# Kernel tuning notes

Measured on AMD Instinct MI355X. Metric: run time of the kernel, lower is better.

The kernel has to match this reference:

```python
import jax, jax.numpy as jnp
import numpy as np
from jax import lax

B, T, C = 4, 1024, 1024
NH, HD = 16, 64
SCALE = 1.0 / np.sqrt(HD)
LN_EPS = 1e-5


def _layernorm(x, g, b):
    mu = jnp.mean(x, axis=-1, keepdims=True)
    var = jnp.var(x, axis=-1, keepdims=True)
    return (x - mu) * lax.rsqrt(var + LN_EPS) * g + b


def _compress(seg, w, g, b):
    # seg: [B, nH, L, hd]; depthwise Conv1d(k=2, s=2, p=1, groups=hd, no bias) + LayerNorm(hd)
    Bs, nH, L, hd = seg.shape
    xc = seg.reshape(Bs * nH, L, hd).transpose(0, 2, 1)  # [B*nH, hd, L]
    y = lax.conv_general_dilated(xc, w, window_strides=(2,), padding=[(1, 1)],
                                 dimension_numbers=('NCH', 'OIH', 'NCH'),
                                 feature_group_count=hd)  # [B*nH, hd, L//2+1]
    y = y.transpose(0, 2, 1)
    y = _layernorm(y, g, b)
    return y.reshape(Bs, nH, -1, hd)


def setup_inputs() -> dict:
    key = jax.random.key(0)
    ks = jax.random.split(key, 16)
    d = {
        'x': jax.random.normal(ks[0], (B, T, C), jnp.float32),
        'mem_k1': jax.random.normal(ks[1], (B, NH, 129, HD), jnp.float32),
        'mem_v1': jax.random.normal(ks[2], (B, NH, 129, HD), jnp.float32),
        'mem_k2': jax.random.normal(ks[3], (B, NH, 257, HD), jnp.float32),
        'mem_v2': jax.random.normal(ks[4], (B, NH, 257, HD), jnp.float32),
        'mem_k3': jax.random.normal(ks[5], (B, NH, 513, HD), jnp.float32),
        'mem_v3': jax.random.normal(ks[6], (B, NH, 513, HD), jnp.float32),
        'c_attn_w': jax.random.normal(ks[7], (3 * C, C), jnp.float32) * 0.02,
        'c_attn_b': jnp.zeros((3 * C,), jnp.float32),
        'c_proj_w': jax.random.normal(ks[8], (C, C), jnp.float32) * 0.02,
        'c_proj_b': jnp.zeros((C,), jnp.float32),
        'compress_k_w': jax.random.normal(ks[9], (HD, 1, 2), jnp.float32) * 0.5,
        'ln_k_g': jnp.ones((HD,), jnp.float32),
        'ln_k_b': jnp.zeros((HD,), jnp.float32),
        'compress_v_w': jax.random.normal(ks[10], (HD, 1, 2), jnp.float32) * 0.5,
        'ln_v_g': jnp.ones((HD,), jnp.float32),
        'ln_v_b': jnp.zeros((HD,), jnp.float32),
    }
    return d


def reference(x, mem_k1, mem_v1, mem_k2, mem_v2, mem_k3, mem_v3,
              c_attn_w, c_attn_b, c_proj_w, c_proj_b,
              compress_k_w, ln_k_g, ln_k_b, compress_v_w, ln_v_g, ln_v_b):
    # qkv projection
    qkv = x @ c_attn_w.T + c_attn_b  # [B, T, 3C]
    q, k_new, v_new = jnp.split(qkv, 3, axis=2)
    q = q.reshape(B, T, NH, HD).transpose(0, 2, 1, 3)       # [B, nH, T, hd]
    k_new = k_new.reshape(B, T, NH, HD).transpose(0, 2, 1, 3)
    v_new = v_new.reshape(B, T, NH, HD).transpose(0, 2, 1, 3)

    # compress the most recent cached segment (513 -> 257)
    k3c = _compress(mem_k3, compress_k_w, ln_k_g, ln_k_b)
    v3c = _compress(mem_v3, compress_v_w, ln_v_g, ln_v_b)

    all_k = jnp.concatenate([mem_k1, mem_k2, k3c, k_new], axis=2)  # [B, nH, T_mem, hd]
    all_v = jnp.concatenate([mem_v1, mem_v2, v3c, v_new], axis=2)
    T_mem = all_k.shape[2]

    att = jnp.einsum('bhqd,bhkd->bhqk', q, all_k) * SCALE  # [B, nH, T, T_mem]
    # causal mask taken from tril(block_size)[:T, :T_mem]: row i attends cols j <= i
    mask = jnp.arange(T)[:, None] >= jnp.arange(T_mem)[None, :]
    att = jnp.where(mask, att, -jnp.inf)
    att = jax.nn.softmax(att, axis=-1)
    y = jnp.einsum('bhqk,bhkd->bhqd', att, all_v)  # [B, nH, T, hd]
    y = y.transpose(0, 2, 1, 3).reshape(B, T, C)
    y = y @ c_proj_w.T + c_proj_b
    return y
```

## Files before the change

### kernel.cpp

```cpp
#include <hip/hip_runtime.h>


using u16    = unsigned short;
using bf16x8 = __attribute__((ext_vector_type(8))) __bf16;
using f32x4  = __attribute__((ext_vector_type(4))) float;
using u16x8  = __attribute__((ext_vector_type(8))) unsigned short;
using u16x4  = __attribute__((ext_vector_type(4))) unsigned short;

__device__ __forceinline__ u16 f2bf(float f) {
    union { float f; unsigned u; } v; v.f = f;
    unsigned r = v.u + 0x7FFFu + ((v.u >> 16) & 1u);
    return (u16)(r >> 16);
}

__device__ __forceinline__ void gload16(const void* src, const void* lds_base) {
    __builtin_amdgcn_global_load_lds(
        (const __attribute__((address_space(1))) void*)src,
        (__attribute__((address_space(3))) void*)lds_base, 16, 0, 0);
}

__global__ void cvt_f32_bf16(const float* __restrict__ src, u16* __restrict__ dst, int n4) {
    int i = blockIdx.x * blockDim.x + threadIdx.x;
    if (i >= n4) return;
    float4 f = reinterpret_cast<const float4*>(src)[i];
    u16x4 o; o[0] = f2bf(f.x); o[1] = f2bf(f.y); o[2] = f2bf(f.z); o[3] = f2bf(f.w);
    reinterpret_cast<u16x4*>(dst)[i] = o;
}

__global__ __launch_bounds__(64) void copy_mem_rows(const float* __restrict__ src,
                                                    u16* __restrict__ dst, int L, int ro) {
    int bh = blockIdx.y, t = blockIdx.x, d = threadIdx.x;
    float v = src[((size_t)bh * L + t) * 64 + d];
    dst[((size_t)bh * 1024 + ro + t) * 64 + d] = f2bf(v);
}

__global__ __launch_bounds__(64) void compress_ln(const float* __restrict__ src,
                                                  const float* __restrict__ w,
                                                  const float* __restrict__ g,
                                                  const float* __restrict__ bta,
                                                  u16* __restrict__ dst, int ro) {
    int bh = blockIdx.y, t = blockIdx.x, d = threadIdx.x;
    const float* seg = src + (size_t)bh * 513 * 64;
    float x0 = (t > 0) ? seg[(size_t)(2 * t - 1) * 64 + d] : 0.f;
    float x1 = seg[(size_t)(2 * t) * 64 + d];
    float y = w[2 * d] * x0 + w[2 * d + 1] * x1;
    float s = y;
    #pragma unroll
    for (int o = 32; o; o >>= 1) s += __shfl_xor(s, o);
    float mu = s * (1.f / 64.f);
    float dv = y - mu;
    float s2 = dv * dv;
    #pragma unroll
    for (int o = 32; o; o >>= 1) s2 += __shfl_xor(s2, o);
    float var = s2 * (1.f / 64.f);
    float out = dv * rsqrtf(var + 1e-5f) * g[d] + bta[d];
    dst[((size_t)bh * 1024 + ro + t) * 64 + d] = f2bf(out);
}

__global__ __launch_bounds__(256) void transpose_v(const u16* __restrict__ src,
                                                   u16* __restrict__ dst) {
    __shared__ u16 tile[64][66];
    const int bh = blockIdx.y, t0 = blockIdx.x * 64;
    const int tid = threadIdx.x;
    #pragma unroll
    for (int i = 0; i < 2; ++i) {
        int p = tid + i * 256;
        int tr = p >> 3, dc = (p & 7) * 8;
        *(u16x8*)&tile[tr][dc] = *(const u16x8*)&src[((size_t)bh * 1024 + t0 + tr) * 64 + dc];
    }
    __syncthreads();
    #pragma unroll
    for (int i = 0; i < 2; ++i) {
        int p = tid + i * 256;
        int d = p >> 3, tc = (p & 7) * 8;
        u16x8 v;
        #pragma unroll
        for (int e = 0; e < 8; ++e) v[e] = tile[tc + e][d];
        *(u16x8*)&dst[((size_t)bh * 64 + d) * 1024 + t0 + tc] = v;
    }
}

__global__ __launch_bounds__(256) void gemm128(const u16* __restrict__ A,
                                               const u16* __restrict__ Bw,
                                               const float* __restrict__ bias,
                                               int K, int N, int mode,
                                               float* __restrict__ outF,
                                               u16* __restrict__ q_buf,
                                               u16* __restrict__ all_k,
                                               u16* __restrict__ all_v) {
    __shared__ __align__(16) u16 Al[2][128 * 32];
    __shared__ __align__(16) u16 Bl[2][128 * 32];
    const int tid = threadIdx.x;
    const int wv = tid >> 6, lane = tid & 63;
    const int lg = lane >> 4, lr = lane & 15;
    const int wr = (wv >> 1) * 64, wc = (wv & 1) * 64;
    const int id = blockIdx.x + blockIdx.y * gridDim.x;
    const int per = (gridDim.x * gridDim.y) >> 3;
    const int nid = (id & 7) * per + (id >> 3);
    const int m0 = (nid % gridDim.x) * 128, n0 = (nid / gridDim.x) * 128;
    f32x4 acc[4][4] = {};
    const int sr0 = tid >> 2,         sc0 = (((tid & 3) << 4)) ^ (((sr0 >> 1) & 3) << 4);
    const int sr1 = (tid + 256) >> 2, sc1 = (((tid & 3) << 4)) ^ (((sr1 >> 1) & 3) << 4);
    const int dA0 = wv * 1024;
    const int dA1 = 4096 + wv * 1024;
    const int nk = K >> 5;
    gload16((const char*)A  + (((size_t)(m0 + sr0) * K) << 1) + sc0, (char*)&Al[0][0] + dA0);
    gload16((const char*)A  + (((size_t)(m0 + sr1) * K) << 1) + sc1, (char*)&Al[0][0] + dA1);
    gload16((const char*)Bw + (((size_t)(n0 + sr0) * K) << 1) + sc0, (char*)&Bl[0][0] + dA0);
    gload16((const char*)Bw + (((size_t)(n0 + sr1) * K) << 1) + sc1, (char*)&Bl[0][0] + dA1);
    __syncthreads();
    int cur = 0;
    for (int kt = 0; kt < nk; ++kt) {
        const char* At = (const char*)&Al[cur][0];
        const char* Bt = (const char*)&Bl[cur][0];
        bf16x8 af[4], bq[4];
        #pragma unroll
        for (int mi = 0; mi < 4; ++mi) {
            int row = wr + mi * 16 + lr;
            af[mi] = *(const bf16x8*)(At + row * 64 + ((lg << 4) ^ (((row >> 1) & 3) << 4)));
        }
        #pragma unroll
        for (int ni = 0; ni < 4; ++ni) {
            int row = wc + ni * 16 + lr;
            bq[ni] = *(const bf16x8*)(Bt + row * 64 + ((lg << 4) ^ (((row >> 1) & 3) << 4)));
        }
        if (kt + 1 < nk) {
            const size_t ko = (size_t)(kt + 1) << 5;
            char* Ad = (char*)&Al[cur ^ 1][0];
            char* Bd = (char*)&Bl[cur ^ 1][0];
            gload16((const char*)A  + (((size_t)(m0 + sr0) * K + ko) << 1) + sc0, Ad + dA0);
            gload16((const char*)A  + (((size_t)(m0 + sr1) * K + ko) << 1) + sc1, Ad + dA1);
            gload16((const char*)Bw + (((size_t)(n0 + sr0) * K + ko) << 1) + sc0, Bd + dA0);
            gload16((const char*)Bw + (((size_t)(n0 + sr1) * K + ko) << 1) + sc1, Bd + dA1);
        }
        __builtin_amdgcn_s_setprio(1);
        #pragma unroll
        for (int mi = 0; mi < 4; ++mi)
            #pragma unroll
            for (int ni = 0; ni < 4; ++ni)
                acc[mi][ni] = __builtin_amdgcn_mfma_f32_16x16x32_bf16(af[mi], bq[ni], acc[mi][ni], 0, 0, 0);
        __builtin_amdgcn_s_setprio(0);
        __syncthreads();
        cur ^= 1;
    }
    #pragma unroll
    for (int mi = 0; mi < 4; ++mi)
        #pragma unroll
        for (int ni = 0; ni < 4; ++ni)
            #pragma unroll
            for (int r = 0; r < 4; ++r) {
                int mm = m0 + wr + mi * 16 + lg * 4 + r;
                int nn = n0 + wc + ni * 16 + lr;
                float v = acc[mi][ni][r] + bias[nn];
                if (mode == 0) {
                    outF[(size_t)mm * N + nn] = v;
                } else {
                    int which = nn >> 10, c = nn & 1023, h = c >> 6, d = c & 63;
                    int b = mm >> 10, t = mm & 1023;
                    int bh = b * 16 + h;
                    if (which == 0) {
                        q_buf[((size_t)bh * 1024 + t) * 64 + d] = f2bf(v * 0.125f);
                    } else if (t < 381) {
                        u16* dst = (which == 1) ? all_k : all_v;
                        dst[((size_t)bh * 1024 + 643 + t) * 64 + d] = f2bf(v);
                    }
                }
            }
}

__global__ __launch_bounds__(256) void attn_kernel(const u16* __restrict__ Q,
                                                   const u16* __restrict__ Kc,
                                                   const u16* __restrict__ VT,
                                                   u16* __restrict__ Y) {
    __shared__ __align__(16) u16 Kl[2][4096];
    __shared__ __align__(16) u16 Vl[2][4096];
    __shared__ __align__(16) u16 P_w[4][16 * 64];
    const int tid = threadIdx.x;
    const int lane = tid & 63;
    const int w = tid >> 6;
    const int lg = lane >> 4, lr = lane & 15;
    const int bh = blockIdx.x;
    const int pair = blockIdx.y;
    const u16* Kb = Kc + (size_t)bh * 65536;
    const u16* Vb = VT + (size_t)bh * 65536;
    char* Pbase = (char*)&P_w[w][0];
    const int xorq = (lr & 7) << 4;

    const int r0 = tid >> 3,         c0 = ((tid & 7) * 16) ^ ((r0 & 7) << 4);
    const int r1 = (tid + 256) >> 3, c1 = ((tid & 7) * 16) ^ ((r1 & 7) << 4);
    const int dst0 = w * 1024;

    for (int phase = 0; phase < 2; ++phase) {
        const int qt = phase ? (15 - pair) : pair;
        const int q0 = qt * 64;
        const u16* Qb = Q + ((size_t)bh * 1024 + q0 + w * 16) * 64;
        bf16x8 qf0 = *(const bf16x8*)&Qb[lr * 64 + lg * 8];
        bf16x8 qf1 = *(const bf16x8*)&Qb[lr * 64 + 32 + lg * 8];
        f32x4 o[4] = {};
        float m = -1e30f, lsum = 0.f;
        const int i_q = q0 + w * 16 + lr;

        {
            const char* Ks = (const char*)Kb;
            gload16(Ks + ((size_t)r0 << 7) + c0, (char*)&Kl[0][0] + dst0);
            gload16(Ks + ((size_t)r1 << 7) + c1, (char*)&Kl[0][0] + 4096 + dst0);
            gload16((const char*)Vb + ((size_t)r0 << 11) + c0, (char*)&Vl[0][0] + dst0);
            gload16((const char*)Vb + ((size_t)r1 << 11) + c1, (char*)&Vl[0][0] + 4096 + dst0);
        }
        __syncthreads();
        int cur = 0;

        for (int kt = 0; kt <= qt; ++kt) {
            if (kt < qt) {
                const int k0n = (kt + 1) * 64;
                const char* Ks = (const char*)Kb + ((size_t)k0n << 7);
                const char* Vs = (const char*)Vb + ((size_t)k0n << 1);
                char* Kd = (char*)&Kl[cur ^ 1][0];
                char* Vd = (char*)&Vl[cur ^ 1][0];
                gload16(Ks + ((size_t)r0 << 7) + c0, Kd + dst0);
                gload16(Ks + ((size_t)r1 << 7) + c1, Kd + 4096 + dst0);
                gload16(Vs + ((size_t)r0 << 11) + c0, Vd + dst0);
                gload16(Vs + ((size_t)r1 << 11) + c1, Vd + 4096 + dst0);
            }
            const char* Kt = (const char*)&Kl[cur][0];
            const char* Vt = (const char*)&Vl[cur][0];
            f32x4 st[4] = {};
            __builtin_amdgcn_s_setprio(1);
            #pragma unroll
            for (int hh = 0; hh < 4; ++hh) {
                const char* Kr = Kt + (size_t)(hh * 16 + lr) * 128;
                bf16x8 kf0 = *(const bf16x8*)(Kr + ((lg * 16) ^ xorq));
                bf16x8 kf1 = *(const bf16x8*)(Kr + ((64 + lg * 16) ^ xorq));
                st[hh] = __builtin_amdgcn_mfma_f32_16x16x32_bf16(kf0, qf0, st[hh], 0, 0, 0);
                st[hh] = __builtin_amdgcn_mfma_f32_16x16x32_bf16(kf1, qf1, st[hh], 0, 0, 0);
            }
            __builtin_amdgcn_s_setprio(0);
            const int k0 = kt * 64;
            float sv[16];
            float tmax = -1e30f;
            if (kt == qt) {
                #pragma unroll
                for (int hh = 0; hh < 4; ++hh)
                    #pragma unroll
                    for (int r = 0; r < 4; ++r) {
                        int j = k0 + hh * 16 + lg * 4 + r;
                        float s = (j <= i_q) ? st[hh][r] : -1e30f;
                        sv[hh * 4 + r] = s;
                        tmax = fmaxf(tmax, s);
                    }
            } else {
                #pragma unroll
                for (int hh = 0; hh < 4; ++hh)
                    #pragma unroll
                    for (int r = 0; r < 4; ++r) {
                        float s = st[hh][r];
                        sv[hh * 4 + r] = s;
                        tmax = fmaxf(tmax, s);
                    }
            }
            tmax = fmaxf(tmax, __shfl_xor(tmax, 16));
            tmax = fmaxf(tmax, __shfl_xor(tmax, 32));
            if (!__all(tmax - m <= 8.f)) {
                float mnew = fmaxf(m, tmax);
                float alpha = __expf(m - mnew);
                #pragma unroll
                for (int c = 0; c < 4; ++c) {
                    o[c][0] *= alpha; o[c][1] *= alpha; o[c][2] *= alpha; o[c][3] *= alpha;
                }
                lsum *= alpha;
                m = mnew;
            }
            float psum = 0.f;
            #pragma unroll
            for (int hh = 0; hh < 4; ++hh) {
                u16x4 pk;
                #pragma unroll
                for (int r = 0; r < 4; ++r) {
                    float p = __expf(sv[hh * 4 + r] - m);
                    psum += p;
                    pk[r] = f2bf(p);
                }
                *(u16x4*)(Pbase + lr * 128 + ((hh * 32 + lg * 8) ^ xorq)) = pk;
            }
            psum += __shfl_xor(psum, 16);
            psum += __shfl_xor(psum, 32);
            lsum += psum;
            asm volatile("s_waitcnt lgkmcnt(0)" ::: "memory");
            __builtin_amdgcn_sched_barrier(0);
            #pragma unroll
            for (int ks = 0; ks < 2; ++ks) {
                bf16x8 pf = *(const bf16x8*)(Pbase + lr * 128 + ((ks * 64 + lg * 16) ^ xorq));
                __builtin_amdgcn_s_setprio(1);
                #pragma unroll
                for (int c = 0; c < 4; ++c) {
                    const char* Vr = Vt + (size_t)(c * 16 + lr) * 128;
                    bf16x8 vf = *(const bf16x8*)(Vr + ((ks * 64 + lg * 16) ^ xorq));
                    o[c] = __builtin_amdgcn_mfma_f32_16x16x32_bf16(vf, pf, o[c], 0, 0, 0);
                }
                __builtin_amdgcn_s_setprio(0);
            }
            __syncthreads();
            cur ^= 1;
        }
        float inv = 1.0f / lsum;
        #pragma unroll
        for (int c = 0; c < 4; ++c) {
            u16x4 ov;
            #pragma unroll
            for (int r = 0; r < 4; ++r) ov[r] = f2bf(o[c][r] * inv);
            *(u16x4*)(Pbase + lr * 128 + (((c * 16 + lg * 4) * 2) ^ xorq)) = ov;
        }
        asm volatile("s_waitcnt lgkmcnt(0)" ::: "memory");
        __builtin_amdgcn_sched_barrier(0);
        const int b = bh >> 4, h = bh & 15;
        const int qr = lane >> 2, dseg = (lane & 3) * 16;
        const int xorr = (qr & 7) << 4;
        size_t g = ((size_t)(b * 1024 + q0 + w * 16 + qr)) * 1024 + h * 64 + dseg;
        *(u16x8*)&Y[g]     = *(const u16x8*)(Pbase + qr * 128 + ((dseg * 2) ^ xorr));
        *(u16x8*)&Y[g + 8] = *(const u16x8*)(Pbase + qr * 128 + ((dseg * 2 + 16) ^ xorr));
    }
}

extern "C" void kernel_launch(void* const* d_in, const int* in_sizes, int n_in,
                              void* d_out, int out_size, void* d_ws, size_t ws_size,
                              hipStream_t stream) {
    const float* x            = (const float*)d_in[0];
    const float* mem_k1       = (const float*)d_in[1];
    const float* mem_v1       = (const float*)d_in[2];
    const float* mem_k2       = (const float*)d_in[3];
    const float* mem_v2       = (const float*)d_in[4];
    const float* mem_k3       = (const float*)d_in[5];
    const float* mem_v3       = (const float*)d_in[6];
    const float* c_attn_w     = (const float*)d_in[7];
    const float* c_attn_b     = (const float*)d_in[8];
    const float* c_proj_w     = (const float*)d_in[9];
    const float* c_proj_b     = (const float*)d_in[10];
    const float* compress_k_w = (const float*)d_in[11];
    const float* ln_k_g       = (const float*)d_in[12];
    const float* ln_k_b       = (const float*)d_in[13];
    const float* compress_v_w = (const float*)d_in[14];
    const float* ln_v_g       = (const float*)d_in[15];
    const float* ln_v_b       = (const float*)d_in[16];

    char* ws = (char*)d_ws;
    u16* x_bf   = (u16*)(ws);
    u16* all_vT = (u16*)(ws);
    u16* wq_bf  = (u16*)(ws + (8u << 20));
    u16* wp_bf  = (u16*)(ws + (14u << 20));
    u16* q_buf  = (u16*)(ws + (16u << 20));
    u16* all_k  = (u16*)(ws + (24u << 20));
    u16* all_v  = (u16*)(ws + (32u << 20));
    u16* att_y  = (u16*)(ws + (40u << 20));
    float* out = (float*)d_out;

    cvt_f32_bf16<<<4096, 256, 0, stream>>>(x, x_bf, 1048576);
    cvt_f32_bf16<<<3072, 256, 0, stream>>>(c_attn_w, wq_bf, 786432);
    cvt_f32_bf16<<<1024, 256, 0, stream>>>(c_proj_w, wp_bf, 262144);

    copy_mem_rows<<<dim3(129, 64), 64, 0, stream>>>(mem_k1, all_k, 129, 0);
    copy_mem_rows<<<dim3(129, 64), 64, 0, stream>>>(mem_v1, all_v, 129, 0);
    copy_mem_rows<<<dim3(257, 64), 64, 0, stream>>>(mem_k2, all_k, 257, 129);
    copy_mem_rows<<<dim3(257, 64), 64, 0, stream>>>(mem_v2, all_v, 257, 129);

    compress_ln<<<dim3(257, 64), 64, 0, stream>>>(mem_k3, compress_k_w, ln_k_g, ln_k_b, all_k, 386);
    compress_ln<<<dim3(257, 64), 64, 0, stream>>>(mem_v3, compress_v_w, ln_v_g, ln_v_b, all_v, 386);

    gemm128<<<dim3(32, 24), 256, 0, stream>>>(x_bf, wq_bf, c_attn_b, 1024, 3072, 1,
                                              nullptr, q_buf, all_k, all_v);

    transpose_v<<<dim3(16, 64), 256, 0, stream>>>(all_v, all_vT);

    attn_kernel<<<dim3(64, 8), 256, 0, stream>>>(q_buf, all_k, all_vT, att_y);

    gemm128<<<dim3(32, 8), 256, 0, stream>>>(att_y, wp_bf, c_proj_b, 1024, 1024, 0,
                                             out, nullptr, nullptr, nullptr);
}
```

Before: 133.0 us.

## Triple-buffer GEMM LDS with fine-grained vmcnt waits and XCD-aware tile mapping

The projection GEMM goes from double to triple buffering in LDS. Loads for tile kt+2 are issued before computing tile kt, and each step waits only on the older loads (vmcnt(4)) with a raw s_barrier in place of __syncthreads. The block-to-tile mapping also changes so each XCD group covers a contiguous 2D region of M and N tiles, which should improve L2 reuse. The cost is 50% more LDS, which may lower occupancy, and hand-written waitcnt logic whose correctness depends on the compiler keeping the load order.

```diff
diff --git a/kernel.cpp b/kernel.cpp
--- a/kernel.cpp
+++ b/kernel.cpp
@@ -88,31 +88,46 @@
                                                u16* __restrict__ q_buf,
                                                u16* __restrict__ all_k,
                                                u16* __restrict__ all_v) {
-    __shared__ __align__(16) u16 Al[2][128 * 32];
-    __shared__ __align__(16) u16 Bl[2][128 * 32];
+    __shared__ __align__(16) u16 Al[3][128 * 32];
+    __shared__ __align__(16) u16 Bl[3][128 * 32];
     const int tid = threadIdx.x;
     const int wv = tid >> 6, lane = tid & 63;
     const int lg = lane >> 4, lr = lane & 15;
     const int wr = (wv >> 1) * 64, wc = (wv & 1) * 64;
     const int id = blockIdx.x + blockIdx.y * gridDim.x;
-    const int per = (gridDim.x * gridDim.y) >> 3;
-    const int nid = (id & 7) * per + (id >> 3);
-    const int m0 = (nid % gridDim.x) * 128, n0 = (nid / gridDim.x) * 128;
+    const int gx = gridDim.x;
+    const int pm = gx >> 2;
+    const int xcd = id & 7, lid = id >> 3;
+    const int mg = xcd >> 1, ng = xcd & 1;
+    const int lm = lid % pm, ln = lid / pm;
+    const int m0 = (mg * pm + lm) * 128;
+    const int n0 = (ng * (gridDim.y >> 1) + ln) * 128;
     f32x4 acc[4][4] = {};
-    const int sr0 = tid >> 2,         sc0 = (((tid & 3) << 4)) ^ (((sr0 >> 1) & 3) << 4);
-    const int sr1 = (tid + 256) >> 2, sc1 = (((tid & 3) << 4)) ^ (((sr1 >> 1) & 3) << 4);
+    const int sr0 = tid >> 2,         sc0 = ((tid & 3) << 4) ^ (((sr0 >> 1) & 3) << 4);
+    const int sr1 = (tid + 256) >> 2, sc1 = ((tid & 3) << 4) ^ (((sr1 >> 1) & 3) << 4);
     const int dA0 = wv * 1024;
     const int dA1 = 4096 + wv * 1024;
     const int nk = K >> 5;
-    gload16((const char*)A  + (((size_t)(m0 + sr0) * K) << 1) + sc0, (char*)&Al[0][0] + dA0);
-    gload16((const char*)A  + (((size_t)(m0 + sr1) * K) << 1) + sc1, (char*)&Al[0][0] + dA1);
-    gload16((const char*)Bw + (((size_t)(n0 + sr0) * K) << 1) + sc0, (char*)&Bl[0][0] + dA0);
-    gload16((const char*)Bw + (((size_t)(n0 + sr1) * K) << 1) + sc1, (char*)&Bl[0][0] + dA1);
-    __syncthreads();
-    int cur = 0;
+
+    auto stage = [&](int j) {
+        const size_t ko = (size_t)j << 5;
+        char* Ad = (char*)&Al[j % 3][0];
+        char* Bd = (char*)&Bl[j % 3][0];
+        gload16((const char*)A  + (((size_t)(m0 + sr0) * K + ko) << 1) + sc0, Ad + dA0);
+        gload16((const char*)A  + (((size_t)(m0 + sr1) * K + ko) << 1) + sc1, Ad + dA1);
+        gload16((const char*)Bw + (((size_t)(n0 + sr0) * K + ko) << 1) + sc0, Bd + dA0);
+        gload16((const char*)Bw + (((size_t)(n0 + sr1) * K + ko) << 1) + sc1, Bd + dA1);
+    };
+    stage(0);
+    stage(1);
+    asm volatile("s_waitcnt vmcnt(4)" ::: "memory");
+    __builtin_amdgcn_s_barrier();
+    __builtin_amdgcn_sched_barrier(0);
+
     for (int kt = 0; kt < nk; ++kt) {
-        const char* At = (const char*)&Al[cur][0];
-        const char* Bt = (const char*)&Bl[cur][0];
+        if (kt + 2 < nk) stage(kt + 2);
+        const char* At = (const char*)&Al[kt % 3][0];
+        const char* Bt = (const char*)&Bl[kt % 3][0];
         bf16x8 af[4], bq[4];
         #pragma unroll
         for (int mi = 0; mi < 4; ++mi) {
@@ -124,15 +139,6 @@
             int row = wc + ni * 16 + lr;
             bq[ni] = *(const bf16x8*)(Bt + row * 64 + ((lg << 4) ^ (((row >> 1) & 3) << 4)));
         }
-        if (kt + 1 < nk) {
-            const size_t ko = (size_t)(kt + 1) << 5;
-            char* Ad = (char*)&Al[cur ^ 1][0];
-            char* Bd = (char*)&Bl[cur ^ 1][0];
-            gload16((const char*)A  + (((size_t)(m0 + sr0) * K + ko) << 1) + sc0, Ad + dA0);
-            gload16((const char*)A  + (((size_t)(m0 + sr1) * K + ko) << 1) + sc1, Ad + dA1);
-            gload16((const char*)Bw + (((size_t)(n0 + sr0) * K + ko) << 1) + sc0, Bd + dA0);
-            gload16((const char*)Bw + (((size_t)(n0 + sr1) * K + ko) << 1) + sc1, Bd + dA1);
-        }
         __builtin_amdgcn_s_setprio(1);
         #pragma unroll
         for (int mi = 0; mi < 4; ++mi)
@@ -140,8 +146,15 @@
             for (int ni = 0; ni < 4; ++ni)
                 acc[mi][ni] = __builtin_amdgcn_mfma_f32_16x16x32_bf16(af[mi], bq[ni], acc[mi][ni], 0, 0, 0);
         __builtin_amdgcn_s_setprio(0);
-        __syncthreads();
-        cur ^= 1;
+        if (kt + 1 < nk) {
+            if (kt + 2 < nk) {
+                asm volatile("s_waitcnt vmcnt(4)" ::: "memory");
+            } else {
+                asm volatile("s_waitcnt vmcnt(0)" ::: "memory");
+            }
+            __builtin_amdgcn_s_barrier();
+            __builtin_amdgcn_sched_barrier(0);
+        }
     }
     #pragma unroll
     for (int mi = 0; mi < 4; ++mi)
```

Result: slower. 139.6 us (+5.0%).

## Merge prep kernels and split-K the output projection GEMM

Applied to the files above, without the earlier changes.

Merges the three fp32-to-bf16 conversions into one launch and the six memory copy/compress launches into one prep kernel, which cuts launch overhead and raises per-block work from 64 to 256 threads. The output projection GEMM now splits K in two, doubling its grid from 256 to 512 blocks to fill more CUs. The two fp32 partial results are then summed with the bias by a new combine kernel. The split path costs extra fp32 partial traffic and one more launch, and it only runs when the workspace is at least 64 MiB; pp1 is placed at 16 MiB, overlapping q_buf, which is safe only because attention has already consumed q_buf.

```diff
diff --git a/kernel.cpp b/kernel.cpp
--- a/kernel.cpp
+++ b/kernel.cpp
@@ -19,42 +19,68 @@
         (__attribute__((address_space(3))) void*)lds_base, 16, 0, 0);
 }
 
-__global__ void cvt_f32_bf16(const float* __restrict__ src, u16* __restrict__ dst, int n4) {
-    int i = blockIdx.x * blockDim.x + threadIdx.x;
-    if (i >= n4) return;
-    float4 f = reinterpret_cast<const float4*>(src)[i];
+__global__ __launch_bounds__(256) void cvt_all(const float* __restrict__ x,
+                                               const float* __restrict__ wa,
+                                               const float* __restrict__ wp,
+                                               u16* __restrict__ xb,
+                                               u16* __restrict__ wab,
+                                               u16* __restrict__ wpb) {
+    int i = blockIdx.x * 256 + threadIdx.x;
+    const float4* s; u16x4* d; int j;
+    if (i < 1048576)      { s = (const float4*)x;  d = (u16x4*)xb;  j = i; }
+    else if (i < 1835008) { s = (const float4*)wa; d = (u16x4*)wab; j = i - 1048576; }
+    else                  { s = (const float4*)wp; d = (u16x4*)wpb; j = i - 1835008; }
+    float4 f = s[j];
     u16x4 o; o[0] = f2bf(f.x); o[1] = f2bf(f.y); o[2] = f2bf(f.z); o[3] = f2bf(f.w);
-    reinterpret_cast<u16x4*>(dst)[i] = o;
-}
-
-__global__ __launch_bounds__(64) void copy_mem_rows(const float* __restrict__ src,
-                                                    u16* __restrict__ dst, int L, int ro) {
-    int bh = blockIdx.y, t = blockIdx.x, d = threadIdx.x;
-    float v = src[((size_t)bh * L + t) * 64 + d];
-    dst[((size_t)bh * 1024 + ro + t) * 64 + d] = f2bf(v);
-}
-
-__global__ __launch_bounds__(64) void compress_ln(const float* __restrict__ src,
-                                                  const float* __restrict__ w,
-                                                  const float* __restrict__ g,
-                                                  const float* __restrict__ bta,
-                                                  u16* __restrict__ dst, int ro) {
-    int bh = blockIdx.y, t = blockIdx.x, d = threadIdx.x;
-    const float* seg = src + (size_t)bh * 513 * 64;
-    float x0 = (t > 0) ? seg[(size_t)(2 * t - 1) * 64 + d] : 0.f;
-    float x1 = seg[(size_t)(2 * t) * 64 + d];
-    float y = w[2 * d] * x0 + w[2 * d + 1] * x1;
-    float s = y;
-    #pragma unroll
-    for (int o = 32; o; o >>= 1) s += __shfl_xor(s, o);
-    float mu = s * (1.f / 64.f);
-    float dv = y - mu;
-    float s2 = dv * dv;
-    #pragma unroll
-    for (int o = 32; o; o >>= 1) s2 += __shfl_xor(s2, o);
-    float var = s2 * (1.f / 64.f);
-    float out = dv * rsqrtf(var + 1e-5f) * g[d] + bta[d];
-    dst[((size_t)bh * 1024 + ro + t) * 64 + d] = f2bf(out);
+    d[j] = o;
+}
+
+__global__ __launch_bounds__(256) void prep_mem(const float* __restrict__ k1,
+                                                const float* __restrict__ v1,
+                                                const float* __restrict__ k2,
+                                                const float* __restrict__ v2,
+                                                const float* __restrict__ k3,
+                                                const float* __restrict__ v3,
+                                                const float* __restrict__ wk,
+                                                const float* __restrict__ gk,
+                                                const float* __restrict__ bk,
+                                                const float* __restrict__ wv,
+                                                const float* __restrict__ gv,
+                                                const float* __restrict__ bv,
+                                                u16* __restrict__ all_k,
+                                                u16* __restrict__ all_v) {
+    const int bh = blockIdx.y;
+    const int ru = blockIdx.x * 4 + (threadIdx.x >> 6);
+    const int d = threadIdx.x & 63;
+    if (ru >= 1286) return;
+    if (ru < 772) {
+        const float* src; u16* dst; int t, ro, L;
+        if (ru < 129)      { t = ru;       src = k1; dst = all_k; ro = 0;   L = 129; }
+        else if (ru < 258) { t = ru - 129; src = v1; dst = all_v; ro = 0;   L = 129; }
+        else if (ru < 515) { t = ru - 258; src = k2; dst = all_k; ro = 129; L = 257; }
+        else               { t = ru - 515; src = v2; dst = all_v; ro = 129; L = 257; }
+        float v = src[((size_t)bh * L + t) * 64 + d];
+        dst[((size_t)bh * 1024 + ro + t) * 64 + d] = f2bf(v);
+    } else {
+        const float* seg; const float* w; const float* g; const float* bta; u16* dst; int t;
+        if (ru < 1029) { t = ru - 772;  seg = k3; w = wk; g = gk; bta = bk; dst = all_k; }
+        else           { t = ru - 1029; seg = v3; w = wv; g = gv; bta = bv; dst = all_v; }
+        const float* sb = seg + (size_t)bh * 513 * 64;
+        float x0 = (t > 0) ? sb[(size_t)(2 * t - 1) * 64 + d] : 0.f;
+        float x1 = sb[(size_t)(2 * t) * 64 + d];
+        float y = w[2 * d] * x0 + w[2 * d + 1] * x1;
+        float s = y;
+        #pragma unroll
+        for (int o = 32; o; o >>= 1) s += __shfl_xor(s, o);
+        float mu = s * (1.f / 64.f);
+        float dv = y - mu;
+        float s2 = dv * dv;
+        #pragma unroll
+        for (int o = 32; o; o >>= 1) s2 += __shfl_xor(s2, o);
+        float var = s2 * (1.f / 64.f);
+        float out = dv * rsqrtf(var + 1e-5f) * g[d] + bta[d];
+        dst[((size_t)bh * 1024 + 386 + t) * 64 + d] = f2bf(out);
+    }
 }
 
 __global__ __launch_bounds__(256) void transpose_v(const u16* __restrict__ src,
@@ -83,8 +109,9 @@
 __global__ __launch_bounds__(256) void gemm128(const u16* __restrict__ A,
                                                const u16* __restrict__ Bw,
                                                const float* __restrict__ bias,
-                                               int K, int N, int mode,
+                                               int K, int N, int mode, int ksplit,
                                                float* __restrict__ outF,
+                                               size_t partStride,
                                                u16* __restrict__ q_buf,
                                                u16* __restrict__ all_k,
                                                u16* __restrict__ all_v) {
@@ -97,17 +124,22 @@
     const int id = blockIdx.x + blockIdx.y * gridDim.x;
     const int per = (gridDim.x * gridDim.y) >> 3;
     const int nid = (id & 7) * per + (id >> 3);
-    const int m0 = (nid % gridDim.x) * 128, n0 = (nid / gridDim.x) * 128;
+    const int m0 = (nid % gridDim.x) * 128;
+    const int rest = nid / gridDim.x;
+    const int nt = rest / ksplit, ks = rest % ksplit;
+    const int n0 = nt * 128;
+    const int Kp = K / ksplit;
+    const int koff = ks * Kp;
     f32x4 acc[4][4] = {};
-    const int sr0 = tid >> 2,         sc0 = (((tid & 3) << 4)) ^ (((sr0 >> 1) & 3) << 4);
-    const int sr1 = (tid + 256) >> 2, sc1 = (((tid & 3) << 4)) ^ (((sr1 >> 1) & 3) << 4);
+    const int sr0 = tid >> 2,         sc0 = ((tid & 3) << 4) ^ (((sr0 >> 1) & 3) << 4);
+    const int sr1 = (tid + 256) >> 2, sc1 = ((tid & 3) << 4) ^ (((sr1 >> 1) & 3) << 4);
     const int dA0 = wv * 1024;
     const int dA1 = 4096 + wv * 1024;
-    const int nk = K >> 5;
-    gload16((const char*)A  + (((size_t)(m0 + sr0) * K) << 1) + sc0, (char*)&Al[0][0] + dA0);
-    gload16((const char*)A  + (((size_t)(m0 + sr1) * K) << 1) + sc1, (char*)&Al[0][0] + dA1);
-    gload16((const char*)Bw + (((size_t)(n0 + sr0) * K) << 1) + sc0, (char*)&Bl[0][0] + dA0);
-    gload16((const char*)Bw + (((size_t)(n0 + sr1) * K) << 1) + sc1, (char*)&Bl[0][0] + dA1);
+    const int nk = Kp >> 5;
+    gload16((const char*)A  + (((size_t)(m0 + sr0) * K + koff) << 1) + sc0, (char*)&Al[0][0] + dA0);
+    gload16((const char*)A  + (((size_t)(m0 + sr1) * K + koff) << 1) + sc1, (char*)&Al[0][0] + dA1);
+    gload16((const char*)Bw + (((size_t)(n0 + sr0) * K + koff) << 1) + sc0, (char*)&Bl[0][0] + dA0);
+    gload16((const char*)Bw + (((size_t)(n0 + sr1) * K + koff) << 1) + sc1, (char*)&Bl[0][0] + dA1);
     __syncthreads();
     int cur = 0;
     for (int kt = 0; kt < nk; ++kt) {
@@ -125,7 +157,7 @@
             bq[ni] = *(const bf16x8*)(Bt + row * 64 + ((lg << 4) ^ (((row >> 1) & 3) << 4)));
         }
         if (kt + 1 < nk) {
-            const size_t ko = (size_t)(kt + 1) << 5;
+            const size_t ko = koff + ((size_t)(kt + 1) << 5);
             char* Ad = (char*)&Al[cur ^ 1][0];
             char* Bd = (char*)&Bl[cur ^ 1][0];
             gload16((const char*)A  + (((size_t)(m0 + sr0) * K + ko) << 1) + sc0, Ad + dA0);
@@ -151,10 +183,12 @@
             for (int r = 0; r < 4; ++r) {
                 int mm = m0 + wr + mi * 16 + lg * 4 + r;
                 int nn = n0 + wc + ni * 16 + lr;
-                float v = acc[mi][ni][r] + bias[nn];
                 if (mode == 0) {
-                    outF[(size_t)mm * N + nn] = v;
+                    outF[(size_t)mm * N + nn] = acc[mi][ni][r] + bias[nn];
+                } else if (mode == 2) {
+                    outF[(size_t)ks * partStride + (size_t)mm * N + nn] = acc[mi][ni][r];
                 } else {
+                    float v = acc[mi][ni][r] + bias[nn];
                     int which = nn >> 10, c = nn & 1023, h = c >> 6, d = c & 63;
                     int b = mm >> 10, t = mm & 1023;
                     int bh = b * 16 + h;
@@ -166,6 +200,20 @@
                     }
                 }
             }
+}
+
+__global__ __launch_bounds__(256) void combine_proj(const float* __restrict__ pp0,
+                                                    const float* __restrict__ pp1,
+                                                    const float* __restrict__ bias,
+                                                    float* __restrict__ out) {
+    int i = blockIdx.x * 256 + threadIdx.x;
+    float4 a = ((const float4*)pp0)[i];
+    float4 b = ((const float4*)pp1)[i];
+    float4 bs = ((const float4*)bias)[i & 255];
+    float4 o;
+    o.x = a.x + b.x + bs.x; o.y = a.y + b.y + bs.y;
+    o.z = a.z + b.z + bs.z; o.w = a.w + b.w + bs.w;
+    ((float4*)out)[i] = o;
 }
 
 __global__ __launch_bounds__(256) void attn_kernel(const u16* __restrict__ Q,
@@ -351,27 +399,32 @@
     u16* all_k  = (u16*)(ws + (24u << 20));
     u16* all_v  = (u16*)(ws + (32u << 20));
     u16* att_y  = (u16*)(ws + (40u << 20));
+    float* pp1  = (float*)(ws + (16u << 20));
+    float* pp0  = (float*)(ws + (48u << 20));
     float* out = (float*)d_out;
 
-    cvt_f32_bf16<<<4096, 256, 0, stream>>>(x, x_bf, 1048576);
-    cvt_f32_bf16<<<3072, 256, 0, stream>>>(c_attn_w, wq_bf, 786432);
-    cvt_f32_bf16<<<1024, 256, 0, stream>>>(c_proj_w, wp_bf, 262144);
-
-    copy_mem_rows<<<dim3(129, 64), 64, 0, stream>>>(mem_k1, all_k, 129, 0);
-    copy_mem_rows<<<dim3(129, 64), 64, 0, stream>>>(mem_v1, all_v, 129, 0);
-    copy_mem_rows<<<dim3(257, 64), 64, 0, stream>>>(mem_k2, all_k, 257, 129);
-    copy_mem_rows<<<dim3(257, 64), 64, 0, stream>>>(mem_v2, all_v, 257, 129);
-
-    compress_ln<<<dim3(257, 64), 64, 0, stream>>>(mem_k3, compress_k_w, ln_k_g, ln_k_b, all_k, 386);
-    compress_ln<<<dim3(257, 64), 64, 0, stream>>>(mem_v3, compress_v_w, ln_v_g, ln_v_b, all_v, 386);
-
-    gemm128<<<dim3(32, 24), 256, 0, stream>>>(x_bf, wq_bf, c_attn_b, 1024, 3072, 1,
-                                              nullptr, q_buf, all_k, all_v);
+    cvt_all<<<8192, 256, 0, stream>>>(x, c_attn_w, c_proj_w, x_bf, wq_bf, wp_bf);
+
+    prep_mem<<<dim3(322, 64), 256, 0, stream>>>(mem_k1, mem_v1, mem_k2, mem_v2,
+                                                mem_k3, mem_v3,
+                                                compress_k_w, ln_k_g, ln_k_b,
+                                                compress_v_w, ln_v_g, ln_v_b,
+                                                all_k, all_v);
+
+    gemm128<<<dim3(32, 24), 256, 0, stream>>>(x_bf, wq_bf, c_attn_b, 1024, 3072, 1, 1,
+                                              nullptr, 0, q_buf, all_k, all_v);
 
     transpose_v<<<dim3(16, 64), 256, 0, stream>>>(all_v, all_vT);
 
     attn_kernel<<<dim3(64, 8), 256, 0, stream>>>(q_buf, all_k, all_vT, att_y);
 
-    gemm128<<<dim3(32, 8), 256, 0, stream>>>(att_y, wp_bf, c_proj_b, 1024, 1024, 0,
-                                             out, nullptr, nullptr, nullptr);
-}
+    if (ws_size >= (64ull << 20)) {
+        size_t stride = (size_t)(pp1 - pp0);
+        gemm128<<<dim3(32, 16), 256, 0, stream>>>(att_y, wp_bf, nullptr, 1024, 1024, 2, 2,
+                                                  pp0, stride, nullptr, nullptr, nullptr);
+        combine_proj<<<4096, 256, 0, stream>>>(pp0, pp0 + stride, c_proj_b, out);
+    } else {
+        gemm128<<<dim3(32, 8), 256, 0, stream>>>(att_y, wp_bf, c_proj_b, 1024, 1024, 0, 1,
+                                                 out, 0, nullptr, nullptr, nullptr);
+    }
+}
```

Result: faster. 128.9 us (-3.0%).
